# Performance work log

Hardware: AMD Instinct MI355X
Metric: run time of the kernel (lower is better)

## Reference

```python
import jax, jax.numpy as jnp
import numpy as np

N_NODES = 100000
N_EDGES = 1600000
NEG_SLOPE = 0.2
EPS = 1e-16


def _add_self_loops(edge_index, n):
    loops = jnp.arange(n, dtype=edge_index.dtype)
    return jnp.concatenate([edge_index, jnp.stack([loops, loops])], axis=1)


def gat_conv(x, edge_index, W, att_src, att_dst, bias, concat):
    """PyG-style GATConv. x:[N,F], W:[F,H*C], att_*:[H,C], bias:[H*C] or [C]."""
    n = x.shape[0]
    heads, ch = att_src.shape
    ei = _add_self_loops(edge_index, n)
    src, dst = ei[0], ei[1]
    h = (x @ W).reshape(n, heads, ch)                    # [N,H,C]
    a_src = jnp.sum(h * att_src[None], axis=-1)          # [N,H]
    a_dst = jnp.sum(h * att_dst[None], axis=-1)          # [N,H]
    alpha = a_src[src] + a_dst[dst]                      # [E,H]
    alpha = jax.nn.leaky_relu(alpha, NEG_SLOPE)
    # edge softmax over destination neighborhoods
    m = jax.ops.segment_max(alpha, dst, num_segments=n)  # [N,H]
    m = jnp.where(jnp.isfinite(m), m, 0.0)
    e = jnp.exp(alpha - m[dst])                          # [E,H]
    s = jax.ops.segment_sum(e, dst, num_segments=n)      # [N,H]
    coef = e / (s[dst] + EPS)                            # [E,H]
    msg = h[src] * coef[:, :, None]                      # [E,H,C]
    out = jax.ops.segment_sum(msg, dst, num_segments=n)  # [N,H,C]
    if concat:
        out = out.reshape(n, heads * ch)
    else:
        out = out.mean(axis=1)
    return out + bias


def setup_inputs() -> dict:
    key = jax.random.key(0)
    ks = jax.random.split(key, 10)
    f_in, hid = 128, 64
    x = jax.random.normal(ks[0], (N_NODES, f_in), dtype=jnp.float32)
    edge_index = jax.random.randint(ks[1], (2, N_EDGES), 0, N_NODES, dtype=jnp.int64)
    sc1 = 1.0 / np.sqrt(f_in)
    sc2 = 1.0 / np.sqrt(2 * hid)
    return {
        "x": x,
        "edge_index": edge_index,
        "W1": jax.random.normal(ks[2], (f_in, 2 * hid), dtype=jnp.float32) * sc1,
        "att_src1": jax.random.normal(ks[3], (2, hid), dtype=jnp.float32) * sc1,
        "att_dst1": jax.random.normal(ks[4], (2, hid), dtype=jnp.float32) * sc1,
        "bias1": jnp.zeros((2 * hid,), dtype=jnp.float32),
        "W2": jax.random.normal(ks[5], (2 * hid, hid), dtype=jnp.float32) * sc2,
        "att_src2": jax.random.normal(ks[6], (1, hid), dtype=jnp.float32) * sc2,
        "att_dst2": jax.random.normal(ks[7], (1, hid), dtype=jnp.float32) * sc2,
        "bias2": jnp.zeros((hid,), dtype=jnp.float32),
    }


def reference(x, edge_index, W1, att_src1, att_dst1, bias1, W2, att_src2, att_dst2, bias2):
    h = gat_conv(x, edge_index, W1, att_src1, att_dst1, bias1, concat=True)
    h = jax.nn.relu(h)
    out = gat_conv(h, edge_index, W2, att_src2, att_dst2, bias2, concat=False)
    return out
```

## Files before the change

kernel.cpp:

```cpp
#include <hip/hip_runtime.h>
#include <hip/hip_bf16.h>
#include <cstdint>
#include <cstddef>

#define LEAKY(x) ((x) > 0.f ? (x) : 0.2f * (x))

#define NBUCK 256
#define BSH   9
#define BPAD  16
#define WPAD  136

typedef float        f32x4  __attribute__((ext_vector_type(4)));
typedef unsigned int u32x4  __attribute__((ext_vector_type(4)));
typedef short        bf16x8 __attribute__((ext_vector_type(8)));

__device__ __forceinline__ float readlane_f(float v, int l) {
    return __int_as_float(__builtin_amdgcn_readlane(__float_as_int(v), l));
}
__device__ __forceinline__ unsigned short f2bf(float f) {
    unsigned x = __float_as_uint(f);
    return (unsigned short)((x + 0x7fffu + ((x >> 16) & 1u)) >> 16);
}
__device__ __forceinline__ float bf_lo(unsigned u) { return __uint_as_float(u << 16); }
__device__ __forceinline__ float bf_hi(unsigned u) { return __uint_as_float(u & 0xffff0000u); }

__device__ __forceinline__ bf16x8 as_bf16x8(u32x4 u) {
    union { u32x4 u4; bf16x8 b; } cv;
    cv.u4 = u;
    return cv.b;
}

__global__ void hist_bucket(const int* __restrict__ ei, int E, int* __restrict__ bcnt,
                            int nblocks) {
    __shared__ int bl[NBUCK];
    for (int i = threadIdx.x; i < NBUCK; i += 256) bl[i] = 0;
    __syncthreads();
    const int stride = nblocks * 256;
    for (int e = blockIdx.x * 256 + threadIdx.x; e < E; e += stride)
        atomicAdd(&bl[ei[E + e] >> BSH], 1);
    __syncthreads();
    for (int i = threadIdx.x; i < NBUCK; i += 256) {
        int c = bl[i];
        if (c) atomicAdd(&bcnt[i * BPAD], c);
    }
}

__global__ void scan_bucket(const int* __restrict__ bcnt, int* __restrict__ bcur,
                            int* __restrict__ bstart, int* __restrict__ offsets, int n) {
    if (threadIdx.x == 0 && blockIdx.x == 0) {
        int run = 0;
        for (int b = 0; b < NBUCK; ++b) {
            int v = bcnt[b * BPAD];
            bcur[b * BPAD] = run;
            bstart[b] = run;
            run += v;
        }
        bstart[NBUCK] = run;
        offsets[n] = run;
    }
}

__global__ __launch_bounds__(256) void fused_gemm1_pass1(
    const float* __restrict__ x, const float* __restrict__ W1, int M,
    const float* __restrict__ att_src, const float* __restrict__ att_dst,
    unsigned* __restrict__ hpk, float* __restrict__ asrc, float* __restrict__ adst,
    const int* __restrict__ ei, int E, int* __restrict__ bcur, int2* __restrict__ ebuf,
    int p1Blocks) {
    const int tid = threadIdx.x;
    if ((int)blockIdx.x < p1Blocks) {
        __shared__ int bcnt_l[NBUCK];
        __shared__ int bbase_l[NBUCK];
        const int e0 = (int)blockIdx.x * 4096;
        const int ecnt = min(4096, E - e0);
        for (int i = tid; i < NBUCK; i += 256) bcnt_l[i] = 0;
        __syncthreads();
        for (int i = tid; i < ecnt; i += 256)
            atomicAdd(&bcnt_l[ei[E + e0 + i] >> BSH], 1);
        __syncthreads();
        if (tid < NBUCK) {
            int c = bcnt_l[tid];
            bbase_l[tid] = c ? atomicAdd(&bcur[tid * BPAD], c) : 0;
            bcnt_l[tid] = 0;
        }
        __syncthreads();
        for (int i = tid; i < ecnt; i += 256) {
            int s = ei[e0 + i];
            int d = ei[E + e0 + i];
            int b = d >> BSH;
            int l = atomicAdd(&bcnt_l[b], 1);
            ebuf[bbase_l[b] + l] = make_int2(s, d);
        }
    } else {
        __shared__ unsigned short Wt[128][WPAD];
        for (int i = tid; i < 128 * 128; i += 256) {
            int k = i >> 7, c = i & 127;
            Wt[c][k] = f2bf(W1[i]);
        }
        __syncthreads();
        const int gb = (int)blockIdx.x - p1Blocks;
        const int lane = tid & 63;
        const int li = lane & 15, g = lane >> 4;
        const int row0 = gb * 64 + (tid >> 6) * 16;
        const int arow = min(row0 + li, M - 1);
        f32x4 acc[8];
#pragma unroll
        for (int ct = 0; ct < 8; ++ct) acc[ct] = (f32x4)(0.f);
        const float* ap = x + (size_t)arow * 128 + g * 8;
#pragma unroll
        for (int ks = 0; ks < 4; ++ks) {
            float4 a0 = *(const float4*)(ap + ks * 32);
            float4 a1 = *(const float4*)(ap + ks * 32 + 4);
            u32x4 af;
            af.x = (unsigned)f2bf(a0.x) | ((unsigned)f2bf(a0.y) << 16);
            af.y = (unsigned)f2bf(a0.z) | ((unsigned)f2bf(a0.w) << 16);
            af.z = (unsigned)f2bf(a1.x) | ((unsigned)f2bf(a1.y) << 16);
            af.w = (unsigned)f2bf(a1.z) | ((unsigned)f2bf(a1.w) << 16);
            bf16x8 av = as_bf16x8(af);
#pragma unroll
            for (int ct = 0; ct < 8; ++ct) {
                bf16x8 bv = *(const bf16x8*)&Wt[ct * 16 + li][ks * 32 + g * 8];
                acc[ct] = __builtin_amdgcn_mfma_f32_16x16x32_bf16(av, bv, acc[ct], 0, 0, 0);
            }
        }
        float asv[8], adv[8];
#pragma unroll
        for (int ct = 0; ct < 8; ++ct) {
            asv[ct] = att_src[ct * 16 + li];
            adv[ct] = att_dst[ct * 16 + li];
        }
#pragma unroll
        for (int reg = 0; reg < 4; ++reg) {
            int r = row0 + g * 4 + reg;
            float ps0 = 0.f, pd0 = 0.f, ps1 = 0.f, pd1 = 0.f;
#pragma unroll
            for (int ct = 0; ct < 4; ++ct) {
                ps0 = fmaf(acc[ct][reg], asv[ct], ps0);
                pd0 = fmaf(acc[ct][reg], adv[ct], pd0);
                ps1 = fmaf(acc[ct + 4][reg], asv[ct + 4], ps1);
                pd1 = fmaf(acc[ct + 4][reg], adv[ct + 4], pd1);
            }
#pragma unroll
            for (int m = 8; m > 0; m >>= 1) {
                ps0 += __shfl_xor(ps0, m);
                pd0 += __shfl_xor(pd0, m);
                ps1 += __shfl_xor(ps1, m);
                pd1 += __shfl_xor(pd1, m);
            }
            if (r < M) {
                if (li == 0) {
                    asrc[2 * r] = ps0; asrc[2 * r + 1] = ps1;
                    adst[2 * r] = pd0; adst[2 * r + 1] = pd1;
                }
#pragma unroll
                for (int ct = 0; ct < 4; ++ct)
                    hpk[(size_t)r * 64 + ct * 16 + li] =
                        (unsigned)f2bf(acc[ct][reg]) | ((unsigned)f2bf(acc[ct + 4][reg]) << 16);
            }
        }
    }
}

__global__ __launch_bounds__(256) void pass2_build(
    const int2* __restrict__ ebuf, const int* __restrict__ bstart, int* __restrict__ offsets,
    int* __restrict__ csr, int N) {
    __shared__ int lcur[1 << BSH];
    __shared__ int ssum[256];
    const int b = blockIdx.x;
    const int dbase = b << BSH;
    const int tid = threadIdx.x;
    for (int i = tid; i < (1 << BSH); i += 256) lcur[i] = 0;
    __syncthreads();
    const int es = bstart[b], ee = bstart[b + 1];
    for (int i = es + tid; i < ee; i += 256)
        atomicAdd(&lcur[ebuf[i].y - dbase], 1);
    __syncthreads();
    const int base_ = tid * 2;
    int v0 = lcur[base_], v1 = lcur[base_ + 1];
    ssum[tid] = v0 + v1;
    __syncthreads();
    for (int o = 1; o < 256; o <<= 1) {
        int add = (tid >= o) ? ssum[tid - o] : 0;
        __syncthreads();
        ssum[tid] += add;
        __syncthreads();
    }
    int excl = (tid ? ssum[tid - 1] : 0) + bstart[b];
    int c0 = excl, c1 = c0 + v0;
    lcur[base_] = c0; lcur[base_ + 1] = c1;
    int idx = dbase + base_;
    if (idx < N)     offsets[idx] = c0;
    if (idx + 1 < N) offsets[idx + 1] = c1;
    __syncthreads();
    for (int i = es + tid; i < ee; i += 256) {
        int2 p = ebuf[i];
        int pos = atomicAdd(&lcur[p.y - dbase], 1);
        csr[pos] = p.x;
    }
}

__global__ __launch_bounds__(256) void gemm2_epi(
    const unsigned short* __restrict__ A, const float* __restrict__ W2, int M,
    const float* __restrict__ att_src, const float* __restrict__ att_dst,
    unsigned short* __restrict__ hb, float* __restrict__ asrc, float* __restrict__ adst) {
    __shared__ unsigned short Wt[64][WPAD];
    const int tid = threadIdx.x;
    for (int i = tid; i < 128 * 64; i += 256) {
        int k = i >> 6, c = i & 63;
        Wt[c][k] = f2bf(W2[i]);
    }
    __syncthreads();
    const int lane = tid & 63;
    const int li = lane & 15, g = lane >> 4;
    const int row0 = blockIdx.x * 64 + (tid >> 6) * 16;
    const int arow = min(row0 + li, M - 1);
    f32x4 acc[4];
#pragma unroll
    for (int ct = 0; ct < 4; ++ct) acc[ct] = (f32x4)(0.f);
    const unsigned short* ap = A + (size_t)arow * 128 + g * 8;
#pragma unroll
    for (int ks = 0; ks < 4; ++ks) {
        bf16x8 av = *(const bf16x8*)(ap + ks * 32);
#pragma unroll
        for (int ct = 0; ct < 4; ++ct) {
            bf16x8 bv = *(const bf16x8*)&Wt[ct * 16 + li][ks * 32 + g * 8];
            acc[ct] = __builtin_amdgcn_mfma_f32_16x16x32_bf16(av, bv, acc[ct], 0, 0, 0);
        }
    }
    float asv[4], adv[4];
#pragma unroll
    for (int ct = 0; ct < 4; ++ct) {
        asv[ct] = att_src[ct * 16 + li];
        adv[ct] = att_dst[ct * 16 + li];
    }
#pragma unroll
    for (int reg = 0; reg < 4; ++reg) {
        int r = row0 + g * 4 + reg;
        float ps = 0.f, pd = 0.f;
#pragma unroll
        for (int ct = 0; ct < 4; ++ct) {
            ps = fmaf(acc[ct][reg], asv[ct], ps);
            pd = fmaf(acc[ct][reg], adv[ct], pd);
        }
#pragma unroll
        for (int m = 8; m > 0; m >>= 1) {
            ps += __shfl_xor(ps, m);
            pd += __shfl_xor(pd, m);
        }
        if (r < M) {
            if (li == 0) { asrc[r] = ps; adst[r] = pd; }
#pragma unroll
            for (int ct = 0; ct < 4; ++ct)
                hb[(size_t)r * 64 + ct * 16 + li] = f2bf(acc[ct][reg]);
        }
    }
}

__global__ void agg_layer1(const unsigned* __restrict__ hpk, const float* __restrict__ asrc,
                           const float* __restrict__ adst, const int* __restrict__ offs,
                           const int* __restrict__ csr, const float* __restrict__ bias,
                           unsigned short* __restrict__ out1b, int N) {
    int node = (blockIdx.x * blockDim.x + threadIdx.x) >> 6;
    int lane = threadIdx.x & 63;
    if (node >= N) return;
    int off = offs[node], end = offs[node + 1];
    float ad0 = adst[2 * node], ad1 = adst[2 * node + 1];
    float ws0 = __expf(fminf(LEAKY(asrc[2 * node] + ad0), 60.f));
    float ws1 = __expf(fminf(LEAKY(asrc[2 * node + 1] + ad1), 60.f));
    float sum0 = ws0, sum1 = ws1;
    float acc0, acc1;
    {
        unsigned u = hpk[(size_t)node * 64 + lane];
        acc0 = ws0 * bf_lo(u);
        acc1 = ws1 * bf_hi(u);
    }
    for (int chunk = off; chunk < end; chunk += 64) {
        int e = chunk + lane;
        int s = 0;
        float w0 = 0.f, w1 = 0.f;
        if (e < end) {
            s = csr[e];
            float2 as = *(const float2*)&asrc[2 * s];
            w0 = __expf(fminf(LEAKY(as.x + ad0), 60.f));
            w1 = __expf(fminf(LEAKY(as.y + ad1), 60.f));
        }
        float t0 = w0, t1 = w1;
#pragma unroll
        for (int o = 32; o > 0; o >>= 1) {
            t0 += __shfl_xor(t0, o);
            t1 += __shfl_xor(t1, o);
        }
        sum0 += t0; sum1 += t1;

        int cnt = min(64, end - chunk);
        int j = 0;
        for (; j + 4 <= cnt; j += 4) {
            int   sj0 = __builtin_amdgcn_readlane(s, j);
            int   sj1 = __builtin_amdgcn_readlane(s, j + 1);
            int   sj2 = __builtin_amdgcn_readlane(s, j + 2);
            int   sj3 = __builtin_amdgcn_readlane(s, j + 3);
            float p0 = readlane_f(w0, j),     q0 = readlane_f(w1, j);
            float p1 = readlane_f(w0, j + 1), q1 = readlane_f(w1, j + 1);
            float p2 = readlane_f(w0, j + 2), q2 = readlane_f(w1, j + 2);
            float p3 = readlane_f(w0, j + 3), q3 = readlane_f(w1, j + 3);
            unsigned u0 = hpk[(size_t)sj0 * 64 + lane];
            unsigned u1 = hpk[(size_t)sj1 * 64 + lane];
            unsigned u2 = hpk[(size_t)sj2 * 64 + lane];
            unsigned u3 = hpk[(size_t)sj3 * 64 + lane];
            acc0 = fmaf(p0, bf_lo(u0), acc0); acc1 = fmaf(q0, bf_hi(u0), acc1);
            acc0 = fmaf(p1, bf_lo(u1), acc0); acc1 = fmaf(q1, bf_hi(u1), acc1);
            acc0 = fmaf(p2, bf_lo(u2), acc0); acc1 = fmaf(q2, bf_hi(u2), acc1);
            acc0 = fmaf(p3, bf_lo(u3), acc0); acc1 = fmaf(q3, bf_hi(u3), acc1);
        }
        for (; j < cnt; ++j) {
            int   sj = __builtin_amdgcn_readlane(s, j);
            float p = readlane_f(w0, j), q = readlane_f(w1, j);
            unsigned u = hpk[(size_t)sj * 64 + lane];
            acc0 = fmaf(p, bf_lo(u), acc0);
            acc1 = fmaf(q, bf_hi(u), acc1);
        }
    }
    float o0 = acc0 / (sum0 + 1e-16f) + bias[lane];
    float o1 = acc1 / (sum1 + 1e-16f) + bias[64 + lane];
    out1b[(size_t)node * 128 + lane]      = f2bf(fmaxf(o0, 0.f));
    out1b[(size_t)node * 128 + 64 + lane] = f2bf(fmaxf(o1, 0.f));
}

__global__ void agg_layer2(const unsigned short* __restrict__ hb, const float* __restrict__ asrc,
                           const float* __restrict__ adst, const int* __restrict__ offs,
                           const int* __restrict__ csr, const float* __restrict__ bias,
                           float* __restrict__ out, int N) {
    int node = (blockIdx.x * blockDim.x + threadIdx.x) >> 6;
    int lane = threadIdx.x & 63;
    if (node >= N) return;
    int off = offs[node], end = offs[node + 1];
    float ad = adst[node];
    float wself = __expf(fminf(LEAKY(asrc[node] + ad), 60.f));
    float sum = wself;
    float acc = wself * __uint_as_float((unsigned)hb[(size_t)node * 64 + lane] << 16);

    for (int chunk = off; chunk < end; chunk += 64) {
        int e = chunk + lane;
        int s = 0;
        float w = 0.f;
        if (e < end) {
            s = csr[e];
            w = __expf(fminf(LEAKY(asrc[s] + ad), 60.f));
        }
        float t = w;
#pragma unroll
        for (int o = 32; o > 0; o >>= 1) t += __shfl_xor(t, o);
        sum += t;

        int cnt = min(64, end - chunk);
        int j = 0;
        for (; j + 4 <= cnt; j += 4) {
            int   sj0 = __builtin_amdgcn_readlane(s, j);
            int   sj1 = __builtin_amdgcn_readlane(s, j + 1);
            int   sj2 = __builtin_amdgcn_readlane(s, j + 2);
            int   sj3 = __builtin_amdgcn_readlane(s, j + 3);
            float p0 = readlane_f(w, j);
            float p1 = readlane_f(w, j + 1);
            float p2 = readlane_f(w, j + 2);
            float p3 = readlane_f(w, j + 3);
            float v0 = __uint_as_float((unsigned)hb[(size_t)sj0 * 64 + lane] << 16);
            float v1 = __uint_as_float((unsigned)hb[(size_t)sj1 * 64 + lane] << 16);
            float v2 = __uint_as_float((unsigned)hb[(size_t)sj2 * 64 + lane] << 16);
            float v3 = __uint_as_float((unsigned)hb[(size_t)sj3 * 64 + lane] << 16);
            acc = fmaf(p0, v0, acc);
            acc = fmaf(p1, v1, acc);
            acc = fmaf(p2, v2, acc);
            acc = fmaf(p3, v3, acc);
        }
        for (; j < cnt; ++j) {
            int   sj = __builtin_amdgcn_readlane(s, j);
            float p = readlane_f(w, j);
            acc = fmaf(p, __uint_as_float((unsigned)hb[(size_t)sj * 64 + lane] << 16), acc);
        }
    }
    out[(size_t)node * 64 + lane] = acc / (sum + 1e-16f) + bias[lane];
}

extern "C" void kernel_launch(void* const* d_in, const int* in_sizes, int n_in,
                              void* d_out, int out_size, void* d_ws, size_t ws_size,
                              hipStream_t stream) {
    const float* x        = (const float*)d_in[0];
    const int* ei         = (const int*)d_in[1];
    const float* W1       = (const float*)d_in[2];
    const float* att_src1 = (const float*)d_in[3];
    const float* att_dst1 = (const float*)d_in[4];
    const float* bias1    = (const float*)d_in[5];
    const float* W2       = (const float*)d_in[6];
    const float* att_src2 = (const float*)d_in[7];
    const float* att_dst2 = (const float*)d_in[8];
    const float* bias2    = (const float*)d_in[9];

    const int N = in_sizes[0] / 128;
    const int E = in_sizes[1] / 2;

    char* base = (char*)d_ws;
    size_t off = 0;
    auto alloc = [&](size_t bytes) {
        char* p = base + off;
        off = (off + bytes + 255) & ~(size_t)255;
        return p;
    };
    int*      bcnt    = (int*)alloc((size_t)NBUCK * BPAD * 4);
    int*      bcur    = (int*)alloc((size_t)NBUCK * BPAD * 4);
    int*      bstart  = (int*)alloc((size_t)(NBUCK + 1) * 4);
    int*      offsets = (int*)alloc((size_t)(N + 1) * 4);
    int*      csr     = (int*)alloc((size_t)E * 4);
    int2*     ebuf    = (int2*)alloc((size_t)E * 8);
    unsigned* hpk     = (unsigned*)alloc((size_t)N * 64 * 4);
    unsigned short* hb    = (unsigned short*)alloc((size_t)N * 64 * 2);
    unsigned short* out1b = (unsigned short*)alloc((size_t)N * 128 * 2);
    float*    asrc1   = (float*)alloc((size_t)N * 2 * 4);
    float*    adst1   = (float*)alloc((size_t)N * 2 * 4);
    float*    asrc2   = (float*)alloc((size_t)N * 4);
    float*    adst2   = (float*)alloc((size_t)N * 4);

    const int mblocks64 = (N + 63) / 64;
    const int nwave_blocks = (N + 3) / 4;
    const int histBlocks = (E + 4095) / 4096;
    const int p1Blocks = (E + 4095) / 4096;
    const int nbuckets = (N + (1 << BSH) - 1) >> BSH;

    hipMemsetAsync(bcnt, 0, (size_t)NBUCK * BPAD * 4, stream);
    hist_bucket<<<histBlocks, 256, 0, stream>>>(ei, E, bcnt, histBlocks);
    scan_bucket<<<1, 64, 0, stream>>>(bcnt, bcur, bstart, offsets, N);

    fused_gemm1_pass1<<<p1Blocks + mblocks64, 256, 0, stream>>>(
        x, W1, N, att_src1, att_dst1, hpk, asrc1, adst1, ei, E, bcur, ebuf, p1Blocks);

    pass2_build<<<nbuckets, 256, 0, stream>>>(ebuf, bstart, offsets, csr, N);

    agg_layer1<<<nwave_blocks, 256, 0, stream>>>(hpk, asrc1, adst1, offsets, csr, bias1, out1b, N);

    gemm2_epi<<<mblocks64, 256, 0, stream>>>(out1b, W2, N, att_src2, att_dst2, hb, asrc2, adst2);

    agg_layer2<<<nwave_blocks, 256, 0, stream>>>(hb, asrc2, adst2, offsets, csr, bias2,
                                                 (float*)d_out, N);
}
```

Baseline: 230.7 us.

## Replace global bucket histogram pass with fixed-capacity per-bucket edge buffers

Removes the separate histogram and scan kernels by giving each destination bucket a fixed-capacity slot region in the edge buffer, filled with per-bucket atomic cursors. Edges that exceed the capacity spill to a small overflow buffer. The build kernel then computes bucket prefixes itself from the final cursor counts. This saves two launches and a full read of the destination indices, at the cost of a larger sparse buffer and an overflow path that is slow and bounded in size. CSR index loads in the aggregation kernels are also switched to nontemporal loads.

```diff
diff --git a/kernel.cpp b/kernel.cpp
--- a/kernel.cpp
+++ b/kernel.cpp
@@ -8,6 +8,7 @@
 #define NBUCK 256
 #define BSH   9
 #define BPAD  16
+#define CAP   16384
 #define WPAD  136
 
 typedef float        f32x4  __attribute__((ext_vector_type(4)));
@@ -28,36 +29,6 @@
     union { u32x4 u4; bf16x8 b; } cv;
     cv.u4 = u;
     return cv.b;
-}
-
-__global__ void hist_bucket(const int* __restrict__ ei, int E, int* __restrict__ bcnt,
-                            int nblocks) {
-    __shared__ int bl[NBUCK];
-    for (int i = threadIdx.x; i < NBUCK; i += 256) bl[i] = 0;
-    __syncthreads();
-    const int stride = nblocks * 256;
-    for (int e = blockIdx.x * 256 + threadIdx.x; e < E; e += stride)
-        atomicAdd(&bl[ei[E + e] >> BSH], 1);
-    __syncthreads();
-    for (int i = threadIdx.x; i < NBUCK; i += 256) {
-        int c = bl[i];
-        if (c) atomicAdd(&bcnt[i * BPAD], c);
-    }
-}
-
-__global__ void scan_bucket(const int* __restrict__ bcnt, int* __restrict__ bcur,
-                            int* __restrict__ bstart, int* __restrict__ offsets, int n) {
-    if (threadIdx.x == 0 && blockIdx.x == 0) {
-        int run = 0;
-        for (int b = 0; b < NBUCK; ++b) {
-            int v = bcnt[b * BPAD];
-            bcur[b * BPAD] = run;
-            bstart[b] = run;
-            run += v;
-        }
-        bstart[NBUCK] = run;
-        offsets[n] = run;
-    }
 }
 
 __global__ __launch_bounds__(256) void fused_gemm1_pass1(
@@ -65,7 +36,7 @@
     const float* __restrict__ att_src, const float* __restrict__ att_dst,
     unsigned* __restrict__ hpk, float* __restrict__ asrc, float* __restrict__ adst,
     const int* __restrict__ ei, int E, int* __restrict__ bcur, int2* __restrict__ ebuf,
-    int p1Blocks) {
+    int2* __restrict__ obuf, int* __restrict__ ocnt, int p1Blocks) {
     const int tid = threadIdx.x;
     if ((int)blockIdx.x < p1Blocks) {
         __shared__ int bcnt_l[NBUCK];
@@ -88,7 +59,13 @@
             int d = ei[E + e0 + i];
             int b = d >> BSH;
             int l = atomicAdd(&bcnt_l[b], 1);
-            ebuf[bbase_l[b] + l] = make_int2(s, d);
+            int g = bbase_l[b] + l;
+            if (g < CAP) {
+                ebuf[(size_t)b * CAP + g] = make_int2(s, d);
+            } else {
+                int oi = atomicAdd(ocnt, 1);
+                obuf[oi & 65535] = make_int2(s, d);
+            }
         }
     } else {
         __shared__ unsigned short Wt[128][WPAD];
@@ -161,18 +138,34 @@
 }
 
 __global__ __launch_bounds__(256) void pass2_build(
-    const int2* __restrict__ ebuf, const int* __restrict__ bstart, int* __restrict__ offsets,
-    int* __restrict__ csr, int N) {
+    const int2* __restrict__ ebuf, const int* __restrict__ bcur,
+    const int2* __restrict__ obuf, const int* __restrict__ ocnt,
+    int* __restrict__ offsets, int* __restrict__ csr, int N, int nbuckets) {
     __shared__ int lcur[1 << BSH];
     __shared__ int ssum[256];
+    __shared__ int cnts[NBUCK];
+    __shared__ int prefix_s;
     const int b = blockIdx.x;
     const int dbase = b << BSH;
     const int tid = threadIdx.x;
+    if (tid < NBUCK) cnts[tid] = (tid < nbuckets) ? bcur[tid * BPAD] : 0;
     for (int i = tid; i < (1 << BSH); i += 256) lcur[i] = 0;
     __syncthreads();
-    const int es = bstart[b], ee = bstart[b + 1];
-    for (int i = es + tid; i < ee; i += 256)
-        atomicAdd(&lcur[ebuf[i].y - dbase], 1);
+    if (tid == 0) {
+        int p = 0;
+        for (int i = 0; i < b; ++i) p += cnts[i];
+        prefix_s = p;
+    }
+    const int tc = cnts[b];
+    const int ec = min(tc, CAP);
+    const int2* eb = ebuf + (size_t)b * CAP;
+    for (int i = tid; i < ec; i += 256)
+        atomicAdd(&lcur[eb[i].y - dbase], 1);
+    const int no = (tc > CAP) ? min(*ocnt, 65536) : 0;
+    for (int i = tid; i < no; i += 256) {
+        int2 p = obuf[i];
+        if ((p.y >> BSH) == b) atomicAdd(&lcur[p.y - dbase], 1);
+    }
     __syncthreads();
     const int base_ = tid * 2;
     int v0 = lcur[base_], v1 = lcur[base_ + 1];
@@ -184,17 +177,25 @@
         ssum[tid] += add;
         __syncthreads();
     }
-    int excl = (tid ? ssum[tid - 1] : 0) + bstart[b];
+    int excl = (tid ? ssum[tid - 1] : 0) + prefix_s;
     int c0 = excl, c1 = c0 + v0;
     lcur[base_] = c0; lcur[base_ + 1] = c1;
     int idx = dbase + base_;
     if (idx < N)     offsets[idx] = c0;
     if (idx + 1 < N) offsets[idx + 1] = c1;
+    if (tid == 0 && b == nbuckets - 1) offsets[N] = prefix_s + tc;
     __syncthreads();
-    for (int i = es + tid; i < ee; i += 256) {
-        int2 p = ebuf[i];
+    for (int i = tid; i < ec; i += 256) {
+        int2 p = eb[i];
         int pos = atomicAdd(&lcur[p.y - dbase], 1);
         csr[pos] = p.x;
+    }
+    for (int i = tid; i < no; i += 256) {
+        int2 p = obuf[i];
+        if ((p.y >> BSH) == b) {
+            int pos = atomicAdd(&lcur[p.y - dbase], 1);
+            csr[pos] = p.x;
+        }
     }
 }
 
@@ -278,7 +279,7 @@
         int s = 0;
         float w0 = 0.f, w1 = 0.f;
         if (e < end) {
-            s = csr[e];
+            s = __builtin_nontemporal_load(&csr[e]);
             float2 as = *(const float2*)&asrc[2 * s];
             w0 = __expf(fminf(LEAKY(as.x + ad0), 60.f));
             w1 = __expf(fminf(LEAKY(as.y + ad1), 60.f));
@@ -343,7 +344,7 @@
         int s = 0;
         float w = 0.f;
         if (e < end) {
-            s = csr[e];
+            s = __builtin_nontemporal_load(&csr[e]);
             w = __expf(fminf(LEAKY(asrc[s] + ad), 60.f));
         }
         float t = w;
@@ -404,12 +405,13 @@
         off = (off + bytes + 255) & ~(size_t)255;
         return p;
     };
-    int*      bcnt    = (int*)alloc((size_t)NBUCK * BPAD * 4);
-    int*      bcur    = (int*)alloc((size_t)NBUCK * BPAD * 4);
-    int*      bstart  = (int*)alloc((size_t)(NBUCK + 1) * 4);
+    const int nbuckets = (N + (1 << BSH) - 1) >> BSH;
+    int*      bcur    = (int*)alloc((size_t)NBUCK * BPAD * 4 + 256);
+    int*      ocnt    = bcur + NBUCK * BPAD;
     int*      offsets = (int*)alloc((size_t)(N + 1) * 4);
     int*      csr     = (int*)alloc((size_t)E * 4);
-    int2*     ebuf    = (int2*)alloc((size_t)E * 8);
+    int2*     ebuf    = (int2*)alloc((size_t)nbuckets * CAP * 8);
+    int2*     obuf    = (int2*)alloc((size_t)65536 * 8);
     unsigned* hpk     = (unsigned*)alloc((size_t)N * 64 * 4);
     unsigned short* hb    = (unsigned short*)alloc((size_t)N * 64 * 2);
     unsigned short* out1b = (unsigned short*)alloc((size_t)N * 128 * 2);
@@ -420,18 +422,15 @@
 
     const int mblocks64 = (N + 63) / 64;
     const int nwave_blocks = (N + 3) / 4;
-    const int histBlocks = (E + 4095) / 4096;
     const int p1Blocks = (E + 4095) / 4096;
-    const int nbuckets = (N + (1 << BSH) - 1) >> BSH;
-
-    hipMemsetAsync(bcnt, 0, (size_t)NBUCK * BPAD * 4, stream);
-    hist_bucket<<<histBlocks, 256, 0, stream>>>(ei, E, bcnt, histBlocks);
-    scan_bucket<<<1, 64, 0, stream>>>(bcnt, bcur, bstart, offsets, N);
+
+    hipMemsetAsync(bcur, 0, (size_t)NBUCK * BPAD * 4 + 256, stream);
 
     fused_gemm1_pass1<<<p1Blocks + mblocks64, 256, 0, stream>>>(
-        x, W1, N, att_src1, att_dst1, hpk, asrc1, adst1, ei, E, bcur, ebuf, p1Blocks);
-
-    pass2_build<<<nbuckets, 256, 0, stream>>>(ebuf, bstart, offsets, csr, N);
+        x, W1, N, att_src1, att_dst1, hpk, asrc1, adst1, ei, E, bcur, ebuf, obuf, ocnt,
+        p1Blocks);
+
+    pass2_build<<<nbuckets, 256, 0, stream>>>(ebuf, bcur, obuf, ocnt, offsets, csr, N, nbuckets);
 
     agg_layer1<<<nwave_blocks, 256, 0, stream>>>(hpk, asrc1, adst1, offsets, csr, bias1, out1b, N);
 
```

Result: faster. 217.8 us (-5.6%).
